# Kernel tuning notes

Measured on AMD Instinct MI355X. Metric: run time of the kernel, lower is better.

## Reference

```python
import jax, jax.numpy as jnp
import numpy as np

B, T, S, H, V, E = 32, 256, 32, 512, 128, 512


def setup_inputs() -> dict:
    key = jax.random.key(0)
    ks = jax.random.split(key, 20)
    f = lambda i, shape: jax.random.normal(ks[i], shape, jnp.float32) * 0.05
    return dict(
        embedding=f(0, (V, H)),
        scope_enc=f(1, (B, S, H)),
        spec_enc=f(2, (B, E)),
        W_init=f(3, (H, E)), b_init=jnp.zeros((H,), jnp.float32),
        W_ih=f(4, (3 * H, 2 * H)), W_hh=f(5, (3 * H, H)),
        b_ih=jnp.zeros((3 * H,), jnp.float32), b_hh=jnp.zeros((3 * H,), jnp.float32),
        W_out=f(6, (V, H)), b_out=jnp.zeros((V,), jnp.float32),
        Wd=f(7, (H, H)), We=f(8, (H, H)), v_attn=f(9, (H,)),
        tokens_in=jax.random.randint(ks[10], (B, T), 0, V),
        tokens_out=jax.random.randint(ks[11], (B, T), 0, V),
        pointer_ids=jax.random.randint(ks[12], (B, T), 0, S),
        ptr_targets=jax.random.randint(ks[13], (B, T), 0, S),
        pointer_mask=jax.random.bernoulli(ks[14], 0.25, (B, T)),
    )


def _gru(x_proj, h0, W_hh, b_hh):
    # x_proj: [B,T,3H] precomputed input projection; torch GRU gate order (r,z,n)
    def step(h, xp):
        gh = h @ W_hh.T + b_hh
        xr, xz, xn = jnp.split(xp, 3, axis=-1)
        hr, hz, hn = jnp.split(gh, 3, axis=-1)
        r = jax.nn.sigmoid(xr + hr)
        z = jax.nn.sigmoid(xz + hz)
        n = jnp.tanh(xn + r * hn)
        h_new = (1.0 - z) * n + z * h
        return h_new, h_new
    _, outs = jax.lax.scan(step, h0, jnp.swapaxes(x_proj, 0, 1))
    return jnp.swapaxes(outs, 0, 1)  # [B,T,H]


def reference(embedding, scope_enc, spec_enc, W_init, b_init, W_ih, W_hh, b_ih, b_hh,
              W_out, b_out, Wd, We, v_attn,
              tokens_in, tokens_out, pointer_ids, ptr_targets, pointer_mask):
    h0 = spec_enc @ W_init.T + b_init                      # initialState
    x_emb = embedding[tokens_in]                           # [B,T,H]
    obj = jax.vmap(lambda s, i: s[i])(scope_enc, pointer_ids)  # [B,T,H]
    obj = jnp.where(pointer_mask[:, :, None], obj, 0.0)    # objectInputs (zeros for non-pointers)
    x = jnp.concatenate([x_emb, obj], axis=-1)             # [B,T,2H]
    x_proj = x @ W_ih.T + b_ih                             # [B,T,3H]
    o = _gru(x_proj, h0, W_hh, b_hh)                       # decoder states [B,T,H]

    # token log-likelihood: -nll_loss(log_softmax(output(o)), targets), summed
    logp = jax.nn.log_softmax(o @ W_out.T + b_out, axis=-1)
    tok_ll = jnp.take_along_axis(logp, tokens_out[:, :, None], axis=-1)[..., 0].sum(-1)

    # pointer attention: additive attention with tanh, log_softmax over scope
    hd = o @ Wd.T                                          # decoderToPointer [B,T,H]
    ok = scope_enc @ We.T                                  # encoderToPointer [B,S,H]
    att = jnp.tanh(hd[:, :, None, :] + ok[:, None, :, :]) @ v_attn  # [B,T,S]
    logatt = jax.nn.log_softmax(att, axis=-1)
    ptr_ll = jnp.take_along_axis(logatt, ptr_targets[:, :, None], axis=-1)[..., 0]
    ptr_ll = jnp.where(pointer_mask, ptr_ll, 0.0).sum(-1)

    return tok_ll + ptr_ll  # per-program likelihood [B]
```

## Files before the change

### kernel.cpp

```cpp
#include <hip/hip_runtime.h>
#include <stdint.h>

#define NB 32
#define NT 256
#define NS 32
#define NH 512
#define NV 128
#define BT 8192

typedef __attribute__((ext_vector_type(8))) __bf16 bf16x8;
typedef __attribute__((ext_vector_type(4))) float f32x4;
typedef __attribute__((ext_vector_type(2))) _Float16 half2v;
typedef unsigned long long u64;

typedef __attribute__((address_space(1))) const unsigned int GASU;
typedef __attribute__((address_space(3))) unsigned int LASU;
#define ASYNC16(g, l) __builtin_amdgcn_global_load_lds((GASU*)(g), (LASU*)(l), 16, 0, 0)

__device__ __forceinline__ half2v pkrtz(float a, float b){
  return __builtin_bit_cast(half2v, __builtin_amdgcn_cvt_pkrtz(a, b));
}
__device__ __forceinline__ unsigned short f2bf(float f){
  unsigned int u = __builtin_bit_cast(unsigned int, f);
  u += 0x7fffu + ((u >> 16) & 1u);
  return (unsigned short)(u >> 16);
}
__device__ __forceinline__ float bf2f(unsigned short h){
  return __builtin_bit_cast(float, ((unsigned int)h) << 16);
}
__device__ __forceinline__ float fexp(float x){ return __builtin_amdgcn_exp2f(x * 1.4426950408889634f); }
__device__ __forceinline__ float fsigm(float x){ return __builtin_amdgcn_rcpf(1.f + fexp(-x)); }
__device__ __forceinline__ float ftanh(float x){
  float t = __builtin_amdgcn_exp2f(x * 2.8853900817779268f);
  return (t - 1.f) * __builtin_amdgcn_rcpf(t + 1.f);
}
__device__ __forceinline__ float flog(float x){ return __builtin_amdgcn_logf(x) * 0.6931471805599453f; }

__device__ __forceinline__ void st_l2(u64* p, u64 v){
  asm volatile("global_store_dwordx2 %0, %1, off" :: "v"(p), "v"(v) : "memory");
}

#define BAR() do{ \
  asm volatile("s_waitcnt lgkmcnt(0)" ::: "memory"); \
  __builtin_amdgcn_sched_barrier(0); \
  __builtin_amdgcn_s_barrier(); \
  __builtin_amdgcn_sched_barrier(0); \
}while(0)

__global__ void k_prep(const float* __restrict__ emb, const float* __restrict__ scope,
                       const float* __restrict__ Wih, const float* __restrict__ Wout,
                       const float* __restrict__ Wd,  const float* __restrict__ We,
                       unsigned short* e_o, unsigned short* s_o, unsigned short* wi_o,
                       unsigned short* wo_o, unsigned short* wd_o, unsigned short* we_o,
                       u64* hx, u64* hxL, float* out, unsigned short* zbuf){
  int g = blockIdx.x*256 + threadIdx.x, gs = gridDim.x*256;
  if (g < 2*NB*256){
    hx[g] = 0ull;
    __hip_atomic_store(hxL + g, 0ull, __ATOMIC_RELAXED, __HIP_MEMORY_SCOPE_AGENT);
  }
  if (g < NB) out[g] = 0.f;
  if (g < 2048) zbuf[g] = 0;
  for (int i=g; i<NV*NH;      i+=gs) e_o[i]  = f2bf(emb[i]);
  for (int i=g; i<NB*NS*NH;   i+=gs) s_o[i]  = f2bf(scope[i]);
  for (int i=g; i<3*NH*2*NH;  i+=gs) wi_o[i] = f2bf(Wih[i]);
  for (int i=g; i<NV*NH;      i+=gs) wo_o[i] = f2bf(Wout[i]);
  for (int i=g; i<NH*NH;      i+=gs) wd_o[i] = f2bf(Wd[i]);
  for (int i=g; i<NH*NH;      i+=gs) we_o[i] = f2bf(We[i]);
}

__global__ void k_h0(const float* __restrict__ spec, const float* __restrict__ Winit,
                     const float* __restrict__ binit, float* __restrict__ h032,
                     u64* __restrict__ hx, u64* __restrict__ hxL){
  const int b = blockIdx.x, tid = threadIdx.x, lane = tid & 63, w = tid >> 6;
  __shared__ float sp[NH];
  __shared__ float hres[NH];
  if (tid < 128) *(float4*)&sp[tid*4] = *(const float4*)(spec + b*NH + tid*4);
  __syncthreads();
  for (int i = 0; i < 128; ++i){
    int j = w * 128 + i;
    const float4* wr = (const float4*)(Winit + (size_t)j * NH);
    float4 x0 = wr[lane*2], x1 = wr[lane*2 + 1];
    float p = x0.x*sp[lane*8]   + x0.y*sp[lane*8+1] + x0.z*sp[lane*8+2] + x0.w*sp[lane*8+3]
            + x1.x*sp[lane*8+4] + x1.y*sp[lane*8+5] + x1.z*sp[lane*8+6] + x1.w*sp[lane*8+7];
    #pragma unroll
    for (int o = 1; o < 64; o <<= 1) p += __shfl_xor(p, o);
    if (lane == 0){
      float v = p + binit[j];
      h032[b*NH + j] = v;
      hres[j] = v;
    }
  }
  __syncthreads();
  if (tid < 256){
    unsigned int pw = __builtin_bit_cast(unsigned int, pkrtz(hres[2*tid], hres[2*tid+1]));
    u64 pv = (1ull << 32) | (u64)pw;
    __hip_atomic_store(hx + b*256 + tid, pv, __ATOMIC_RELAXED, __HIP_MEMORY_SCOPE_AGENT);
    __hip_atomic_store(hxL + b*256 + tid, pv, __ATOMIC_RELAXED, __HIP_MEMORY_SCOPE_AGENT);
  }
}

struct GatherArgs {
  const int* tok; const int* pid; const int* msk;
  const unsigned short* emb; const unsigned short* scope; const unsigned short* zbuf;
};

template<int ASRC>
__global__ __launch_bounds__(256, 2) void k_gemm(
    const unsigned short* __restrict__ A, const unsigned short* __restrict__ Bw,
    float* __restrict__ Cf, unsigned short* __restrict__ Cbf,
    const float* __restrict__ bias, int M, int N, int K, GatherArgs ga)
{
  __shared__ unsigned short lA[2][128][64];
  __shared__ unsigned short lB[2][128][64];
  const int tid = threadIdx.x, lane = tid & 63, wv = tid >> 6;
  const int m0 = blockIdx.x * 128, n0 = blockIdx.y * 128;

  const unsigned short* srcA[4];
  const unsigned short* srcO[4];
  const unsigned short* srcB[4];
  #pragma unroll
  for (int i = 0; i < 4; ++i){
    int ar = m0 + wv*32 + i*8 + (lane >> 3);
    int chunk = (lane & 7) * 8;
    if (ASRC == 0){
      srcA[i] = A + (size_t)ar * K + chunk;
      srcO[i] = nullptr;
    } else {
      int tk = ga.tok[ar], pd = ga.pid[ar], mk = ga.msk[ar];
      srcA[i] = ga.emb + (size_t)tk * NH + chunk;
      srcO[i] = mk ? (ga.scope + ((size_t)((ar >> 8) * NS + pd)) * NH + chunk)
                   : (ga.zbuf + chunk);
    }
    int br = n0 + wv*32 + i*8 + (lane >> 3);
    srcB[i] = Bw + (size_t)br * K + chunk;
  }

  f32x4 acc[4][4];
  #pragma unroll
  for (int x=0;x<4;++x)
    #pragma unroll
    for (int y=0;y<4;++y) acc[x][y] = (f32x4){0.f,0.f,0.f,0.f};

  auto STAGE = [&](int bf, int kt){
    const int k0 = kt * 64;
    #pragma unroll
    for (int i = 0; i < 4; ++i){
      const unsigned short* pa;
      if (ASRC == 0) pa = srcA[i] + k0;
      else pa = (k0 < NH) ? (srcA[i] + k0) : (srcO[i] + (k0 - NH));
      ASYNC16(pa, &lA[bf][wv*32 + i*8][0]);
      ASYNC16(srcB[i] + k0, &lB[bf][wv*32 + i*8][0]);
    }
  };

  STAGE(0, 0);
  asm volatile("s_waitcnt vmcnt(0)" ::: "memory");
  __syncthreads();

  const int wm = (wv >> 1) * 64, wn = (wv & 1) * 64;
  const int fr = lane & 15, fq = lane >> 4;
  const int nt = K >> 6;
  int cur = 0;
  for (int kt = 0; kt < nt; ++kt){
    if (kt + 1 < nt) STAGE(cur ^ 1, kt + 1);
    #pragma unroll
    for (int ks = 0; ks < 2; ++ks){
      bf16x8 af[4], bfv[4];
      #pragma unroll
      for (int mi = 0; mi < 4; ++mi)
        af[mi] = *(const bf16x8*)&lA[cur][wm + mi*16 + fr][ks*32 + fq*8];
      #pragma unroll
      for (int ni = 0; ni < 4; ++ni)
        bfv[ni] = *(const bf16x8*)&lB[cur][wn + ni*16 + fr][ks*32 + fq*8];
      #pragma unroll
      for (int mi = 0; mi < 4; ++mi)
        #pragma unroll
        for (int ni = 0; ni < 4; ++ni)
          acc[mi][ni] = __builtin_amdgcn_mfma_f32_16x16x32_bf16(af[mi], bfv[ni], acc[mi][ni], 0, 0, 0);
    }
    asm volatile("s_waitcnt vmcnt(0)" ::: "memory");
    __syncthreads();
    cur ^= 1;
  }

  #pragma unroll
  for (int mi = 0; mi < 4; ++mi){
    #pragma unroll
    for (int ni = 0; ni < 4; ++ni){
      int col = n0 + wn + ni*16 + fr;
      float bv = bias ? bias[col] : 0.f;
      #pragma unroll
      for (int rr = 0; rr < 4; ++rr){
        int row = m0 + wm + mi*16 + fq*4 + rr;
        float v = acc[mi][ni][rr] + bv;
        if (Cbf) Cbf[(size_t)row * N + col] = f2bf(v);
        else     Cf [(size_t)row * N + col] = v;
      }
    }
  }
}

__global__ __launch_bounds__(512, 1) void k_gru(
    const float* __restrict__ Whh, const float* __restrict__ bhh,
    const unsigned short* __restrict__ xp,
    const float* __restrict__ h032,
    u64* __restrict__ hx,
    u64* __restrict__ hxL,
    unsigned short* __restrict__ obf)
{
  const int bid = blockIdx.x;
  const int b = bid & 31, s = bid >> 5;
  const int tid = threadIdx.x;
  const int u = tid >> 3, r = tid & 7;
  const int jg = s * 64 + u;

  __shared__ __align__(16) unsigned int hl[256];
  __shared__ float xpl[192];
  __shared__ unsigned int pkb[32];

  half2v w0[8][4], w1[8][4], w2[8][4];
  #pragma unroll
  for (int c = 0; c < 8; ++c){
    const int kb = r*64 + ((c + r) & 7) * 8;
    const float* p0 = Whh + ((size_t)(       jg)) * NH + kb;
    const float* p1 = Whh + ((size_t)(  NH + jg)) * NH + kb;
    const float* p2 = Whh + ((size_t)(2*NH + jg)) * NH + kb;
    #pragma unroll
    for (int p = 0; p < 4; ++p){
      float2 a = *(const float2*)(p0 + 2*p);
      float2 c2 = *(const float2*)(p1 + 2*p);
      float2 d = *(const float2*)(p2 + 2*p);
      w0[c][p] = pkrtz(a.x, a.y);
      w1[c][p] = pkrtz(c2.x, c2.y);
      w2[c][p] = pkrtz(d.x, d.y);
    }
  }
  const float bh0 = bhh[jg], bh1 = bhh[NH + jg], bh2 = bhh[2*NH + jg];
  float hprev = h032[b*NH + jg];

  unsigned short xpv = 0;
  if (tid >= 256 && tid < 448){
    int idx = tid - 256;
    xpv = xp[((size_t)(b*NT + 0)) * 1536 + (idx >> 6) * NH + s*64 + (idx & 63)];
  }
  __syncthreads();

  for (int t = 0; t < NT; ++t){
    if (tid < 256){
      const int base = (((t & 1) * NB + b) << 8) + tid;
      const u64* pL = hxL + base;
      const u64* pM = hx + base;
      const unsigned int want = (unsigned int)(t + 1);
      u64 v;
      u64 a  = __hip_atomic_load(pL, __ATOMIC_RELAXED, __HIP_MEMORY_SCOPE_AGENT);
      u64 b2 = __hip_atomic_load(pL, __ATOMIC_RELAXED, __HIP_MEMORY_SCOPE_AGENT);
      int it = 0;
      while (true){
        if ((unsigned int)(a >> 32) == want){ v = a; break; }
        a = b2;
        b2 = __hip_atomic_load(pL, __ATOMIC_RELAXED, __HIP_MEMORY_SCOPE_AGENT);
        if (((++it) & 7) == 0){
          u64 m = __hip_atomic_load(pM, __ATOMIC_RELAXED, __HIP_MEMORY_SCOPE_AGENT);
          if ((unsigned int)(m >> 32) == want){ v = m; break; }
        }
      }
      hl[tid] = (unsigned int)v;
    } else if (tid < 448){
      int idx = tid - 256;
      xpl[idx] = bf2f(xpv);
      if (t + 1 < NT)
        xpv = xp[((size_t)(b*NT + t + 1)) * 1536 + (idx >> 6) * NH + s*64 + (idx & 63)];
    }
    BAR();

    float a0 = 0.f, a1 = 0.f, a2 = 0.f;
    half2v hch[8][4];
    #pragma unroll
    for (int c = 0; c < 8; ++c){
      const int g = (r << 3) + ((c + r) & 7);
      uint4 hv = *(const uint4*)&hl[g * 4];
      hch[c][0] = __builtin_bit_cast(half2v, hv.x);
      hch[c][1] = __builtin_bit_cast(half2v, hv.y);
      hch[c][2] = __builtin_bit_cast(half2v, hv.z);
      hch[c][3] = __builtin_bit_cast(half2v, hv.w);
    }
    #pragma unroll
    for (int c = 0; c < 8; ++c){
      #pragma unroll
      for (int p = 0; p < 4; ++p){
        a0 = __builtin_amdgcn_fdot2(w0[c][p], hch[c][p], a0, false);
        a1 = __builtin_amdgcn_fdot2(w1[c][p], hch[c][p], a1, false);
        a2 = __builtin_amdgcn_fdot2(w2[c][p], hch[c][p], a2, false);
      }
    }
    a0 += __shfl_xor(a0, 1); a0 += __shfl_xor(a0, 2); a0 += __shfl_xor(a0, 4);
    a1 += __shfl_xor(a1, 1); a1 += __shfl_xor(a1, 2); a1 += __shfl_xor(a1, 4);
    a2 += __shfl_xor(a2, 1); a2 += __shfl_xor(a2, 2); a2 += __shfl_xor(a2, 4);

    float hnew = 0.f;
    if (r == 0){
      float xr = xpl[u], xz = xpl[64 + u], xn = xpl[128 + u];
      float rg = fsigm(xr + a0 + bh0);
      float zg = fsigm(xz + a1 + bh1);
      float ng = ftanh(xn + rg * (a2 + bh2));
      hnew = (1.f - zg) * ng + zg * hprev;
      hprev = hnew;
    }
    float hpart = __shfl_xor(hnew, 8);
    if (r == 0 && (u & 1) == 0){
      unsigned int pw = __builtin_bit_cast(unsigned int, pkrtz(hnew, hpart));
      u64 pv = ((u64)(unsigned int)(t + 2) << 32) | (u64)pw;
      const int dst = ((((t + 1) & 1) * NB + b) << 8) + (s << 5) + (u >> 1);
      st_l2(hxL + dst, pv);
      __hip_atomic_store(hx + dst, pv,
                         __ATOMIC_RELAXED, __HIP_MEMORY_SCOPE_AGENT);
      pkb[u >> 1] = (unsigned int)f2bf(hnew) | ((unsigned int)f2bf(hpart) << 16);
    }
    BAR();

    if (tid >= 448 && tid < 480){
      int i = tid - 448;
      ((unsigned int*)obf)[((size_t)(b*NT + t)) * (NH/2) + s*32 + i] = pkb[i];
    }
  }
}

__global__ void k_tokll(const float* __restrict__ logits, const int* __restrict__ tko,
                        float* __restrict__ out){
  const int tid = threadIdx.x, lane = tid & 63, w = tid >> 6;
  const int r0 = blockIdx.x * 64 + w * 16;
  const int b = r0 >> 8;
  int mytok = 0; float tval = 0.f;
  if (lane < 16){
    mytok = tko[r0 + lane];
    tval = logits[(size_t)(r0 + lane) * NV + mytok];
  }
  float acc = 0.f;
  for (int i = 0; i < 16; ++i){
    const float* L = logits + (size_t)(r0 + i) * NV;
    float l0 = L[lane], l1 = L[64 + lane];
    float m = fmaxf(l0, l1);
    #pragma unroll
    for (int o = 1; o < 64; o <<= 1) m = fmaxf(m, __shfl_xor(m, o));
    float sm = fexp(l0 - m) + fexp(l1 - m);
    #pragma unroll
    for (int o = 1; o < 64; o <<= 1) sm += __shfl_xor(sm, o);
    float lse = m + flog(sm);
    float tv = __shfl(tval, i);
    if (lane == 0) acc += tv - lse;
  }
  if (lane == 0) atomicAdd(out + b, acc);
}

__global__ __launch_bounds__(256, 2) void k_ptr(
    const unsigned short* __restrict__ hd, const float* __restrict__ okp,
    const float* __restrict__ vat, const int* __restrict__ ptg,
    const int* __restrict__ pmask, float* __restrict__ out)
{
  __shared__ unsigned short okl[NS][518];
  __shared__ unsigned short hdl[16][518];
  __shared__ float vl[NH];
  __shared__ float attl[16][33];
  const int tid = threadIdx.x;
  const int b = blockIdx.x >> 4, t0 = (blockIdx.x & 15) * 16;
  for (int ii = 0; ii < 64; ++ii){
    int lin = ii*256 + tid;
    int s = lin >> 9, h = lin & 511;
    okl[s][h] = f2bf(okp[((size_t)(b*NS + s)) * NH + h]);
  }
  for (int ii = 0; ii < 32; ++ii){
    int lin = ii*256 + tid;
    int tt = lin >> 9, h = lin & 511;
    hdl[tt][h] = hd[((size_t)(b*NT + t0 + tt)) * NH + h];
  }
  vl[tid] = vat[tid]; vl[256 + tid] = vat[256 + tid];
  __syncthreads();
  #pragma unroll
  for (int pp = 0; pp < 2; ++pp){
    int p = pp*256 + tid;
    int tt = p >> 5, s = p & 31;
    float a = 0.f;
    #pragma unroll 4
    for (int h = 0; h < NH; ++h)
      a += vl[h] * ftanh(bf2f(hdl[tt][h]) + bf2f(okl[s][h]));
    attl[tt][s] = a;
  }
  __syncthreads();
  if (tid < 16){
    int tt = tid;
    float m = -1e30f;
    for (int s = 0; s < NS; ++s) m = fmaxf(m, attl[tt][s]);
    float sm = 0.f;
    for (int s = 0; s < NS; ++s) sm += fexp(attl[tt][s] - m);
    float lse = m + flog(sm);
    int g = b*NT + t0 + tt;
    float c = pmask[g] ? (attl[tt][ptg[g]] - lse) : 0.f;
    #pragma unroll
    for (int o = 1; o < 16; o <<= 1) c += __shfl_xor(c, o);
    if (tid == 0) atomicAdd(out + b, c);
  }
}

extern "C" void kernel_launch(void* const* d_in, const int* in_sizes, int n_in,
                              void* d_out, int out_size, void* d_ws, size_t ws_size,
                              hipStream_t stream)
{
  (void)in_sizes; (void)n_in; (void)out_size; (void)ws_size;
  const float* embedding  = (const float*)d_in[0];
  const float* scope_enc  = (const float*)d_in[1];
  const float* spec_enc   = (const float*)d_in[2];
  const float* W_init     = (const float*)d_in[3];
  const float* b_init     = (const float*)d_in[4];
  const float* W_ih       = (const float*)d_in[5];
  const float* W_hh       = (const float*)d_in[6];
  const float* b_ih       = (const float*)d_in[7];
  const float* b_hh       = (const float*)d_in[8];
  const float* W_out      = (const float*)d_in[9];
  const float* b_out      = (const float*)d_in[10];
  const float* Wd         = (const float*)d_in[11];
  const float* We         = (const float*)d_in[12];
  const float* v_attn     = (const float*)d_in[13];
  const int* tokens_in    = (const int*)d_in[14];
  const int* tokens_out   = (const int*)d_in[15];
  const int* pointer_ids  = (const int*)d_in[16];
  const int* ptr_targets  = (const int*)d_in[17];
  const int* pointer_mask = (const int*)d_in[18];
  float* outF = (float*)d_out;

  uint8_t* wp = (uint8_t*)d_ws;
  auto carve = [&](size_t bytes)->void*{
    void* p = (void*)wp; wp += (bytes + 255) & ~(size_t)255; return p;
  };
  unsigned short* xp_bf    = (unsigned short*)carve((size_t)BT*1536*2);
  unsigned short* o_bf     = (unsigned short*)carve((size_t)BT*NH*2);
  float*          logitsF  = (float*)carve((size_t)BT*NV*4);
  unsigned short* hd_bf    = (unsigned short*)carve((size_t)BT*NH*2);
  float*          okp      = (float*)carve((size_t)NB*NS*NH*4);
  unsigned short* emb_bf   = (unsigned short*)carve((size_t)NV*NH*2);
  unsigned short* scope_bf = (unsigned short*)carve((size_t)NB*NS*NH*2);
  unsigned short* Wih_bf   = (unsigned short*)carve((size_t)3*NH*2*NH*2);
  unsigned short* Wout_bf  = (unsigned short*)carve((size_t)NV*NH*2);
  unsigned short* Wd_bf    = (unsigned short*)carve((size_t)NH*NH*2);
  unsigned short* We_bf    = (unsigned short*)carve((size_t)NH*NH*2);
  float*          h032     = (float*)carve((size_t)NB*NH*4);
  u64*            hx       = (u64*)carve((size_t)2*NB*256*8);
  u64*            hxL      = (u64*)carve((size_t)2*NB*256*8);
  unsigned short* zbuf     = (unsigned short*)carve(4096);

  hipLaunchKernelGGL(k_prep, dim3(1024), dim3(256), 0, stream,
                     embedding, scope_enc, W_ih, W_out, Wd, We,
                     emb_bf, scope_bf, Wih_bf, Wout_bf, Wd_bf, We_bf,
                     hx, hxL, outF, zbuf);
  hipLaunchKernelGGL(k_h0, dim3(NB), dim3(256), 0, stream, spec_enc, W_init, b_init,
                     h032, hx, hxL);
  GatherArgs ga{tokens_in, pointer_ids, pointer_mask, emb_bf, scope_bf, zbuf};
  GatherArgs g0{nullptr,nullptr,nullptr,nullptr,nullptr,nullptr};
  hipLaunchKernelGGL((k_gemm<1>), dim3(64,12), dim3(256), 0, stream,
                     (const unsigned short*)nullptr, Wih_bf, (float*)nullptr, xp_bf,
                     b_ih, BT, 1536, 1024, ga);
  hipLaunchKernelGGL(k_gru, dim3(256), dim3(512), 0, stream,
                     W_hh, b_hh, xp_bf, h032, hx, hxL, o_bf);
  hipLaunchKernelGGL((k_gemm<0>), dim3(64,1), dim3(256), 0, stream,
                     o_bf, Wout_bf, logitsF, (unsigned short*)nullptr, b_out, BT, NV, NH, g0);
  hipLaunchKernelGGL((k_gemm<0>), dim3(64,4), dim3(256), 0, stream,
                     o_bf, Wd_bf, (float*)nullptr, hd_bf, (const float*)nullptr, BT, NH, NH, g0);
  hipLaunchKernelGGL((k_gemm<0>), dim3(8,4), dim3(256), 0, stream,
                     scope_bf, We_bf, okp, (unsigned short*)nullptr, (const float*)nullptr,
                     NB*NS, NH, NH, g0);
  hipLaunchKernelGGL(k_tokll, dim3(128), dim3(256), 0, stream, logitsF, tokens_out, outF);
  hipLaunchKernelGGL(k_ptr, dim3(512), dim3(256), 0, stream,
                     hd_bf, okp, v_attn, ptr_targets, pointer_mask, outF);
}
```

Measured before the change: 646.0 us.

## Fuse input-projection GEMM into GRU kernel with per-row-block ready flags

Merges the gathered input-projection GEMM and the GRU recurrence into one persistent launch. Blocks 0-255 run the GRU and blocks 256+ compute xp tiles, using producer/consumer warp specialisation inside each tile. GRU blocks spin on per-row-block ready counters, so each batch can start once its first half of timesteps is projected, and it waits for the second half at t=127. This aims to hide the GEMM behind the recurrence and drop a launch boundary. It relies on all 1024 blocks being co-resident, otherwise spinning GRU blocks could starve the GEMM blocks and deadlock.

Measured after the change: 803.6 us. 1.24x slower.

```diff
diff --git a/kernel.cpp b/kernel.cpp
--- a/kernel.cpp
+++ b/kernel.cpp
@@ -47,17 +47,23 @@
   __builtin_amdgcn_sched_barrier(0); \
 }while(0)
 
+struct GatherArgs {
+  const int* tok; const int* pid; const int* msk;
+  const unsigned short* emb; const unsigned short* scope; const unsigned short* zbuf;
+};
+
 __global__ void k_prep(const float* __restrict__ emb, const float* __restrict__ scope,
                        const float* __restrict__ Wih, const float* __restrict__ Wout,
                        const float* __restrict__ Wd,  const float* __restrict__ We,
                        unsigned short* e_o, unsigned short* s_o, unsigned short* wi_o,
                        unsigned short* wo_o, unsigned short* wd_o, unsigned short* we_o,
-                       u64* hx, u64* hxL, float* out, unsigned short* zbuf){
+                       u64* hx, u64* hxL, int* ready, float* out, unsigned short* zbuf){
   int g = blockIdx.x*256 + threadIdx.x, gs = gridDim.x*256;
   if (g < 2*NB*256){
     hx[g] = 0ull;
     __hip_atomic_store(hxL + g, 0ull, __ATOMIC_RELAXED, __HIP_MEMORY_SCOPE_AGENT);
   }
+  if (g < 128) __hip_atomic_store(ready + g, 0, __ATOMIC_RELAXED, __HIP_MEMORY_SCOPE_AGENT);
   if (g < NB) out[g] = 0.f;
   if (g < 2048) zbuf[g] = 0;
   for (int i=g; i<NV*NH;      i+=gs) e_o[i]  = f2bf(emb[i]);
@@ -99,124 +105,125 @@
   }
 }
 
-struct GatherArgs {
-  const int* tok; const int* pid; const int* msk;
-  const unsigned short* emb; const unsigned short* scope; const unsigned short* zbuf;
-};
-
-template<int ASRC>
-__global__ __launch_bounds__(256, 2) void k_gemm(
-    const unsigned short* __restrict__ A, const unsigned short* __restrict__ Bw,
-    float* __restrict__ Cf, unsigned short* __restrict__ Cbf,
-    const float* __restrict__ bias, int M, int N, int K, GatherArgs ga)
+__global__ __launch_bounds__(512, 4) void k_main(
+    const float* __restrict__ Whh, const float* __restrict__ bhh,
+    unsigned short* __restrict__ xp,
+    const float* __restrict__ h032,
+    u64* __restrict__ hx, u64* __restrict__ hxL,
+    unsigned short* __restrict__ obf,
+    const unsigned short* __restrict__ Wih,
+    const float* __restrict__ bih,
+    GatherArgs ga, int* __restrict__ ready)
 {
   __shared__ unsigned short lA[2][128][64];
   __shared__ unsigned short lB[2][128][64];
-  const int tid = threadIdx.x, lane = tid & 63, wv = tid >> 6;
-  const int m0 = blockIdx.x * 128, n0 = blockIdx.y * 128;
-
-  const unsigned short* srcA[4];
-  const unsigned short* srcO[4];
-  const unsigned short* srcB[4];
-  #pragma unroll
-  for (int i = 0; i < 4; ++i){
-    int ar = m0 + wv*32 + i*8 + (lane >> 3);
-    int chunk = (lane & 7) * 8;
-    if (ASRC == 0){
-      srcA[i] = A + (size_t)ar * K + chunk;
-      srcO[i] = nullptr;
-    } else {
-      int tk = ga.tok[ar], pd = ga.pid[ar], mk = ga.msk[ar];
-      srcA[i] = ga.emb + (size_t)tk * NH + chunk;
-      srcO[i] = mk ? (ga.scope + ((size_t)((ar >> 8) * NS + pd)) * NH + chunk)
-                   : (ga.zbuf + chunk);
-    }
-    int br = n0 + wv*32 + i*8 + (lane >> 3);
-    srcB[i] = Bw + (size_t)br * K + chunk;
-  }
-
-  f32x4 acc[4][4];
-  #pragma unroll
-  for (int x=0;x<4;++x)
-    #pragma unroll
-    for (int y=0;y<4;++y) acc[x][y] = (f32x4){0.f,0.f,0.f,0.f};
-
-  auto STAGE = [&](int bf, int kt){
-    const int k0 = kt * 64;
-    #pragma unroll
-    for (int i = 0; i < 4; ++i){
-      const unsigned short* pa;
-      if (ASRC == 0) pa = srcA[i] + k0;
-      else pa = (k0 < NH) ? (srcA[i] + k0) : (srcO[i] + (k0 - NH));
-      ASYNC16(pa, &lA[bf][wv*32 + i*8][0]);
-      ASYNC16(srcB[i] + k0, &lB[bf][wv*32 + i*8][0]);
-    }
-  };
-
-  STAGE(0, 0);
-  asm volatile("s_waitcnt vmcnt(0)" ::: "memory");
-  __syncthreads();
-
-  const int wm = (wv >> 1) * 64, wn = (wv & 1) * 64;
-  const int fr = lane & 15, fq = lane >> 4;
-  const int nt = K >> 6;
-  int cur = 0;
-  for (int kt = 0; kt < nt; ++kt){
-    if (kt + 1 < nt) STAGE(cur ^ 1, kt + 1);
-    #pragma unroll
-    for (int ks = 0; ks < 2; ++ks){
-      bf16x8 af[4], bfv[4];
-      #pragma unroll
-      for (int mi = 0; mi < 4; ++mi)
-        af[mi] = *(const bf16x8*)&lA[cur][wm + mi*16 + fr][ks*32 + fq*8];
-      #pragma unroll
-      for (int ni = 0; ni < 4; ++ni)
-        bfv[ni] = *(const bf16x8*)&lB[cur][wn + ni*16 + fr][ks*32 + fq*8];
-      #pragma unroll
-      for (int mi = 0; mi < 4; ++mi)
-        #pragma unroll
-        for (int ni = 0; ni < 4; ++ni)
-          acc[mi][ni] = __builtin_amdgcn_mfma_f32_16x16x32_bf16(af[mi], bfv[ni], acc[mi][ni], 0, 0, 0);
-    }
-    asm volatile("s_waitcnt vmcnt(0)" ::: "memory");
-    __syncthreads();
-    cur ^= 1;
-  }
-
-  #pragma unroll
-  for (int mi = 0; mi < 4; ++mi){
-    #pragma unroll
-    for (int ni = 0; ni < 4; ++ni){
-      int col = n0 + wn + ni*16 + fr;
-      float bv = bias ? bias[col] : 0.f;
-      #pragma unroll
-      for (int rr = 0; rr < 4; ++rr){
-        int row = m0 + wm + mi*16 + fq*4 + rr;
-        float v = acc[mi][ni][rr] + bv;
-        if (Cbf) Cbf[(size_t)row * N + col] = f2bf(v);
-        else     Cf [(size_t)row * N + col] = v;
-      }
-    }
-  }
-}
-
-__global__ __launch_bounds__(512, 1) void k_gru(
-    const float* __restrict__ Whh, const float* __restrict__ bhh,
-    const unsigned short* __restrict__ xp,
-    const float* __restrict__ h032,
-    u64* __restrict__ hx,
-    u64* __restrict__ hxL,
-    unsigned short* __restrict__ obf)
-{
-  const int bid = blockIdx.x;
-  const int b = bid & 31, s = bid >> 5;
-  const int tid = threadIdx.x;
-  const int u = tid >> 3, r = tid & 7;
-  const int jg = s * 64 + u;
-
   __shared__ __align__(16) unsigned int hl[256];
   __shared__ float xpl[192];
   __shared__ unsigned int pkb[32];
+  __shared__ int gDone;
+
+  const int bid = blockIdx.x;
+  const int tid = threadIdx.x;
+  const int lane = tid & 63;
+
+  if (bid >= 256){
+    const int tile = bid - 256;
+    const int rbo = tile / 12, colb = tile - rbo * 12;
+    const int rb = (rbo < 32) ? (rbo << 1) : (((rbo - 32) << 1) | 1);
+    const int m0 = rb << 7, n0 = colb << 7;
+    const int wva = tid >> 6;
+    if (tid == 0) gDone = 0;
+    __syncthreads();
+
+    if (wva >= 4){
+      const int wv = wva - 4;
+      const unsigned short *sA[4], *sO[4], *sB[4];
+      #pragma unroll
+      for (int i = 0; i < 4; ++i){
+        int ar = m0 + wv*32 + i*8 + (lane >> 3);
+        int ch = (lane & 7) * 8;
+        int tk = ga.tok[ar], pd = ga.pid[ar], mk = ga.msk[ar];
+        sA[i] = ga.emb + (size_t)tk * NH + ch;
+        sO[i] = mk ? (ga.scope + ((size_t)((ar >> 8) * NS + pd)) * NH + ch)
+                   : (ga.zbuf + ch);
+        int br = n0 + wv*32 + i*8 + (lane >> 3);
+        sB[i] = Wih + (size_t)br * 1024 + ch;
+      }
+      auto STG = [&](int bf, int kt){
+        const int k0 = kt << 6;
+        #pragma unroll
+        for (int i = 0; i < 4; ++i){
+          const unsigned short* pa = (k0 < NH) ? (sA[i] + k0) : (sO[i] + (k0 - NH));
+          ASYNC16(pa, &lA[bf][wv*32 + i*8][0]);
+          ASYNC16(sB[i] + k0, &lB[bf][wv*32 + i*8][0]);
+        }
+      };
+      STG(0, 0);
+      asm volatile("s_waitcnt vmcnt(0)" ::: "memory");
+      __syncthreads();
+      int cur = 0;
+      for (int kt = 0; kt < 16; ++kt){
+        if (kt < 15) STG(cur ^ 1, kt + 1);
+        asm volatile("s_waitcnt vmcnt(0)" ::: "memory");
+        __syncthreads();
+        cur ^= 1;
+      }
+    } else {
+      f32x4 acc[4][4];
+      #pragma unroll
+      for (int x=0;x<4;++x)
+        #pragma unroll
+        for (int y=0;y<4;++y) acc[x][y] = (f32x4){0.f,0.f,0.f,0.f};
+      __syncthreads();
+      const int wm = (wva >> 1) * 64, wn = (wva & 1) * 64;
+      const int fr = lane & 15, fq = lane >> 4;
+      int cur = 0;
+      for (int kt = 0; kt < 16; ++kt){
+        #pragma unroll
+        for (int ks = 0; ks < 2; ++ks){
+          bf16x8 af[4], bfv[4];
+          #pragma unroll
+          for (int mi = 0; mi < 4; ++mi)
+            af[mi] = *(const bf16x8*)&lA[cur][wm + mi*16 + fr][ks*32 + fq*8];
+          #pragma unroll
+          for (int ni = 0; ni < 4; ++ni)
+            bfv[ni] = *(const bf16x8*)&lB[cur][wn + ni*16 + fr][ks*32 + fq*8];
+          #pragma unroll
+          for (int mi = 0; mi < 4; ++mi)
+            #pragma unroll
+            for (int ni = 0; ni < 4; ++ni)
+              acc[mi][ni] = __builtin_amdgcn_mfma_f32_16x16x32_bf16(af[mi], bfv[ni], acc[mi][ni], 0, 0, 0);
+        }
+        __syncthreads();
+        cur ^= 1;
+      }
+      #pragma unroll
+      for (int mi = 0; mi < 4; ++mi){
+        #pragma unroll
+        for (int ni = 0; ni < 4; ++ni){
+          int col = n0 + wn + ni*16 + fr;
+          float bv = bih[col];
+          #pragma unroll
+          for (int rr = 0; rr < 4; ++rr){
+            int row = m0 + wm + mi*16 + fq*4 + rr;
+            xp[(size_t)row * 1536 + col] = f2bf(acc[mi][ni][rr] + bv);
+          }
+        }
+      }
+      asm volatile("s_waitcnt vmcnt(0)" ::: "memory");
+    }
+    if (lane == 0){
+      if (atomicAdd(&gDone, 1) == 7){
+        __threadfence();
+        atomicAdd(ready + rb, 1);
+      }
+    }
+    return;
+  }
+
+  const int b = bid & 31, s = bid >> 5;
+  const int u = tid >> 3, r = tid & 7;
+  const int jg = s * 64 + u;
 
   half2v w0[8][4], w1[8][4], w2[8][4];
   #pragma unroll
@@ -237,6 +244,12 @@
   }
   const float bh0 = bhh[jg], bh1 = bhh[NH + jg], bh2 = bhh[2*NH + jg];
   float hprev = h032[b*NH + jg];
+
+  if (tid == 0){
+    while (__hip_atomic_load(ready + 2*b, __ATOMIC_RELAXED, __HIP_MEMORY_SCOPE_AGENT) < 12)
+      __builtin_amdgcn_s_sleep(2);
+  }
+  __syncthreads();
 
   unsigned short xpv = 0;
   if (tid >= 256 && tid < 448){
@@ -268,6 +281,10 @@
     } else if (tid < 448){
       int idx = tid - 256;
       xpl[idx] = bf2f(xpv);
+      if (t == 127){
+        while (__hip_atomic_load(ready + 2*b + 1, __ATOMIC_RELAXED,
+                                 __HIP_MEMORY_SCOPE_AGENT) < 12) { }
+      }
       if (t + 1 < NT)
         xpv = xp[((size_t)(b*NT + t + 1)) * 1536 + (idx >> 6) * NH + s*64 + (idx & 63)];
     }
@@ -321,6 +338,90 @@
     if (tid >= 448 && tid < 480){
       int i = tid - 448;
       ((unsigned int*)obf)[((size_t)(b*NT + t)) * (NH/2) + s*32 + i] = pkb[i];
+    }
+  }
+}
+
+template<int ASRC>
+__global__ __launch_bounds__(256, 2) void k_gemm(
+    const unsigned short* __restrict__ A, const unsigned short* __restrict__ Bw,
+    float* __restrict__ Cf, unsigned short* __restrict__ Cbf,
+    const float* __restrict__ bias, int M, int N, int K, GatherArgs ga)
+{
+  __shared__ unsigned short lA[2][128][64];
+  __shared__ unsigned short lB[2][128][64];
+  const int tid = threadIdx.x, lane = tid & 63, wv = tid >> 6;
+  const int m0 = blockIdx.x * 128, n0 = blockIdx.y * 128;
+
+  const unsigned short* srcA[4];
+  const unsigned short* srcB[4];
+  #pragma unroll
+  for (int i = 0; i < 4; ++i){
+    int ar = m0 + wv*32 + i*8 + (lane >> 3);
+    int chunk = (lane & 7) * 8;
+    srcA[i] = A + (size_t)ar * K + chunk;
+    int br = n0 + wv*32 + i*8 + (lane >> 3);
+    srcB[i] = Bw + (size_t)br * K + chunk;
+  }
+
+  f32x4 acc[4][4];
+  #pragma unroll
+  for (int x=0;x<4;++x)
+    #pragma unroll
+    for (int y=0;y<4;++y) acc[x][y] = (f32x4){0.f,0.f,0.f,0.f};
+
+  auto STAGE = [&](int bf, int kt){
+    const int k0 = kt * 64;
+    #pragma unroll
+    for (int i = 0; i < 4; ++i){
+      ASYNC16(srcA[i] + k0, &lA[bf][wv*32 + i*8][0]);
+      ASYNC16(srcB[i] + k0, &lB[bf][wv*32 + i*8][0]);
+    }
+  };
+
+  STAGE(0, 0);
+  asm volatile("s_waitcnt vmcnt(0)" ::: "memory");
+  __syncthreads();
+
+  const int wm = (wv >> 1) * 64, wn = (wv & 1) * 64;
+  const int fr = lane & 15, fq = lane >> 4;
+  const int nt = K >> 6;
+  int cur = 0;
+  for (int kt = 0; kt < nt; ++kt){
+    if (kt + 1 < nt) STAGE(cur ^ 1, kt + 1);
+    #pragma unroll
+    for (int ks = 0; ks < 2; ++ks){
+      bf16x8 af[4], bfv[4];
+      #pragma unroll
+      for (int mi = 0; mi < 4; ++mi)
+        af[mi] = *(const bf16x8*)&lA[cur][wm + mi*16 + fr][ks*32 + fq*8];
+      #pragma unroll
+      for (int ni = 0; ni < 4; ++ni)
+        bfv[ni] = *(const bf16x8*)&lB[cur][wn + ni*16 + fr][ks*32 + fq*8];
+      #pragma unroll
+      for (int mi = 0; mi < 4; ++mi)
+        #pragma unroll
+        for (int ni = 0; ni < 4; ++ni)
+          acc[mi][ni] = __builtin_amdgcn_mfma_f32_16x16x32_bf16(af[mi], bfv[ni], acc[mi][ni], 0, 0, 0);
+    }
+    asm volatile("s_waitcnt vmcnt(0)" ::: "memory");
+    __syncthreads();
+    cur ^= 1;
+  }
+
+  #pragma unroll
+  for (int mi = 0; mi < 4; ++mi){
+    #pragma unroll
+    for (int ni = 0; ni < 4; ++ni){
+      int col = n0 + wn + ni*16 + fr;
+      float bv = bias ? bias[col] : 0.f;
+      #pragma unroll
+      for (int rr = 0; rr < 4; ++rr){
+        int row = m0 + wm + mi*16 + fq*4 + rr;
+        float v = acc[mi][ni][rr] + bv;
+        if (Cbf) Cbf[(size_t)row * N + col] = f2bf(v);
+        else     Cf [(size_t)row * N + col] = v;
+      }
     }
   }
 }
@@ -445,21 +546,19 @@
   float*          h032     = (float*)carve((size_t)NB*NH*4);
   u64*            hx       = (u64*)carve((size_t)2*NB*256*8);
   u64*            hxL      = (u64*)carve((size_t)2*NB*256*8);
+  int*            ready    = (int*)carve(1024);
   unsigned short* zbuf     = (unsigned short*)carve(4096);
 
   hipLaunchKernelGGL(k_prep, dim3(1024), dim3(256), 0, stream,
                      embedding, scope_enc, W_ih, W_out, Wd, We,
                      emb_bf, scope_bf, Wih_bf, Wout_bf, Wd_bf, We_bf,
-                     hx, hxL, outF, zbuf);
+                     hx, hxL, ready, outF, zbuf);
   hipLaunchKernelGGL(k_h0, dim3(NB), dim3(256), 0, stream, spec_enc, W_init, b_init,
                      h032, hx, hxL);
   GatherArgs ga{tokens_in, pointer_ids, pointer_mask, emb_bf, scope_bf, zbuf};
   GatherArgs g0{nullptr,nullptr,nullptr,nullptr,nullptr,nullptr};
-  hipLaunchKernelGGL((k_gemm<1>), dim3(64,12), dim3(256), 0, stream,
-                     (const unsigned short*)nullptr, Wih_bf, (float*)nullptr, xp_bf,
-                     b_ih, BT, 1536, 1024, ga);
-  hipLaunchKernelGGL(k_gru, dim3(256), dim3(512), 0, stream,
-                     W_hh, b_hh, xp_bf, h032, hx, hxL, o_bf);
+  hipLaunchKernelGGL(k_main, dim3(1024), dim3(512), 0, stream,
+                     W_hh, b_hh, xp_bf, h032, hx, hxL, o_bf, Wih_bf, b_ih, ga, ready);
   hipLaunchKernelGGL((k_gemm<0>), dim3(64,1), dim3(256), 0, stream,
                      o_bf, Wout_bf, logitsF, (unsigned short*)nullptr, b_out, BT, NV, NH, g0);
   hipLaunchKernelGGL((k_gemm<0>), dim3(64,4), dim3(256), 0, stream,
```

## Precompute input projections per vocab row and scope row instead of per token

Applied to the files above, without the earlier changes.

The input projection x @ W_ih^T is split into an embedding part and a pointer-object part. Each part is projected once over the small tables (128 vocab rows and 1024 scope rows), replacing the 8192-row gathered GEMM. The GRU kernel then gathers the projected rows per timestep by token and pointer id and adds them, using the mask to drop the object term. This removes a large GEMM and its 8192x1536 intermediate, but adds two dependent index loads and an extra add per step inside the latency-critical recurrence.

Result: faster. 596.6 us (-7.6%).

```diff
diff --git a/kernel.cpp b/kernel.cpp
--- a/kernel.cpp
+++ b/kernel.cpp
@@ -52,14 +52,13 @@
                        const float* __restrict__ Wd,  const float* __restrict__ We,
                        unsigned short* e_o, unsigned short* s_o, unsigned short* wi_o,
                        unsigned short* wo_o, unsigned short* wd_o, unsigned short* we_o,
-                       u64* hx, u64* hxL, float* out, unsigned short* zbuf){
+                       u64* hx, u64* hxL, float* out){
   int g = blockIdx.x*256 + threadIdx.x, gs = gridDim.x*256;
   if (g < 2*NB*256){
     hx[g] = 0ull;
     __hip_atomic_store(hxL + g, 0ull, __ATOMIC_RELAXED, __HIP_MEMORY_SCOPE_AGENT);
   }
   if (g < NB) out[g] = 0.f;
-  if (g < 2048) zbuf[g] = 0;
   for (int i=g; i<NV*NH;      i+=gs) e_o[i]  = f2bf(emb[i]);
   for (int i=g; i<NB*NS*NH;   i+=gs) s_o[i]  = f2bf(scope[i]);
   for (int i=g; i<3*NH*2*NH;  i+=gs) wi_o[i] = f2bf(Wih[i]);
@@ -99,16 +98,10 @@
   }
 }
 
-struct GatherArgs {
-  const int* tok; const int* pid; const int* msk;
-  const unsigned short* emb; const unsigned short* scope; const unsigned short* zbuf;
-};
-
-template<int ASRC>
 __global__ __launch_bounds__(256, 2) void k_gemm(
     const unsigned short* __restrict__ A, const unsigned short* __restrict__ Bw,
     float* __restrict__ Cf, unsigned short* __restrict__ Cbf,
-    const float* __restrict__ bias, int M, int N, int K, GatherArgs ga)
+    const float* __restrict__ bias, int M, int N, int K, int ldb)
 {
   __shared__ unsigned short lA[2][128][64];
   __shared__ unsigned short lB[2][128][64];
@@ -116,23 +109,14 @@
   const int m0 = blockIdx.x * 128, n0 = blockIdx.y * 128;
 
   const unsigned short* srcA[4];
-  const unsigned short* srcO[4];
   const unsigned short* srcB[4];
   #pragma unroll
   for (int i = 0; i < 4; ++i){
     int ar = m0 + wv*32 + i*8 + (lane >> 3);
     int chunk = (lane & 7) * 8;
-    if (ASRC == 0){
-      srcA[i] = A + (size_t)ar * K + chunk;
-      srcO[i] = nullptr;
-    } else {
-      int tk = ga.tok[ar], pd = ga.pid[ar], mk = ga.msk[ar];
-      srcA[i] = ga.emb + (size_t)tk * NH + chunk;
-      srcO[i] = mk ? (ga.scope + ((size_t)((ar >> 8) * NS + pd)) * NH + chunk)
-                   : (ga.zbuf + chunk);
-    }
+    srcA[i] = A + (size_t)ar * K + chunk;
     int br = n0 + wv*32 + i*8 + (lane >> 3);
-    srcB[i] = Bw + (size_t)br * K + chunk;
+    srcB[i] = Bw + (size_t)br * ldb + chunk;
   }
 
   f32x4 acc[4][4];
@@ -145,10 +129,7 @@
     const int k0 = kt * 64;
     #pragma unroll
     for (int i = 0; i < 4; ++i){
-      const unsigned short* pa;
-      if (ASRC == 0) pa = srcA[i] + k0;
-      else pa = (k0 < NH) ? (srcA[i] + k0) : (srcO[i] + (k0 - NH));
-      ASYNC16(pa, &lA[bf][wv*32 + i*8][0]);
+      ASYNC16(srcA[i] + k0, &lA[bf][wv*32 + i*8][0]);
       ASYNC16(srcB[i] + k0, &lB[bf][wv*32 + i*8][0]);
     }
   };
@@ -202,7 +183,10 @@
 
 __global__ __launch_bounds__(512, 1) void k_gru(
     const float* __restrict__ Whh, const float* __restrict__ bhh,
-    const unsigned short* __restrict__ xp,
+    const unsigned short* __restrict__ embp,
+    const unsigned short* __restrict__ objp,
+    const int* __restrict__ tokin, const int* __restrict__ pids,
+    const int* __restrict__ pmask,
     const float* __restrict__ h032,
     u64* __restrict__ hx,
     u64* __restrict__ hxL,
@@ -238,10 +222,16 @@
   const float bh0 = bhh[jg], bh1 = bhh[NH + jg], bh2 = bhh[2*NH + jg];
   float hprev = h032[b*NH + jg];
 
-  unsigned short xpv = 0;
+  unsigned short xe = 0, xo = 0; int mk = 0;
+  int jcol = 0;
   if (tid >= 256 && tid < 448){
     int idx = tid - 256;
-    xpv = xp[((size_t)(b*NT + 0)) * 1536 + (idx >> 6) * NH + s*64 + (idx & 63)];
+    jcol = (idx >> 6) * NH + s*64 + (idx & 63);
+    int tk = tokin[b*NT + 0];
+    int pd = pids [b*NT + 0];
+    mk     = pmask[b*NT + 0];
+    xe = embp[(size_t)tk * 1536 + jcol];
+    xo = objp[((size_t)(b*NS + pd)) * 1536 + jcol];
   }
   __syncthreads();
 
@@ -267,9 +257,14 @@
       hl[tid] = (unsigned int)v;
     } else if (tid < 448){
       int idx = tid - 256;
-      xpl[idx] = bf2f(xpv);
-      if (t + 1 < NT)
-        xpv = xp[((size_t)(b*NT + t + 1)) * 1536 + (idx >> 6) * NH + s*64 + (idx & 63)];
+      xpl[idx] = bf2f(xe) + (mk ? bf2f(xo) : 0.f);
+      if (t + 1 < NT){
+        int tk = tokin[b*NT + t + 1];
+        int pd = pids [b*NT + t + 1];
+        mk     = pmask[b*NT + t + 1];
+        xe = embp[(size_t)tk * 1536 + jcol];
+        xo = objp[((size_t)(b*NS + pd)) * 1536 + jcol];
+      }
     }
     BAR();
 
@@ -431,7 +426,8 @@
   auto carve = [&](size_t bytes)->void*{
     void* p = (void*)wp; wp += (bytes + 255) & ~(size_t)255; return p;
   };
-  unsigned short* xp_bf    = (unsigned short*)carve((size_t)BT*1536*2);
+  unsigned short* embp_bf  = (unsigned short*)carve((size_t)NV*1536*2);
+  unsigned short* objp_bf  = (unsigned short*)carve((size_t)NB*NS*1536*2);
   unsigned short* o_bf     = (unsigned short*)carve((size_t)BT*NH*2);
   float*          logitsF  = (float*)carve((size_t)BT*NV*4);
   unsigned short* hd_bf    = (unsigned short*)carve((size_t)BT*NH*2);
@@ -445,28 +441,31 @@
   float*          h032     = (float*)carve((size_t)NB*NH*4);
   u64*            hx       = (u64*)carve((size_t)2*NB*256*8);
   u64*            hxL      = (u64*)carve((size_t)2*NB*256*8);
-  unsigned short* zbuf     = (unsigned short*)carve(4096);
 
   hipLaunchKernelGGL(k_prep, dim3(1024), dim3(256), 0, stream,
                      embedding, scope_enc, W_ih, W_out, Wd, We,
                      emb_bf, scope_bf, Wih_bf, Wout_bf, Wd_bf, We_bf,
-                     hx, hxL, outF, zbuf);
+                     hx, hxL, outF);
   hipLaunchKernelGGL(k_h0, dim3(NB), dim3(256), 0, stream, spec_enc, W_init, b_init,
                      h032, hx, hxL);
-  GatherArgs ga{tokens_in, pointer_ids, pointer_mask, emb_bf, scope_bf, zbuf};
-  GatherArgs g0{nullptr,nullptr,nullptr,nullptr,nullptr,nullptr};
-  hipLaunchKernelGGL((k_gemm<1>), dim3(64,12), dim3(256), 0, stream,
-                     (const unsigned short*)nullptr, Wih_bf, (float*)nullptr, xp_bf,
-                     b_ih, BT, 1536, 1024, ga);
+  hipLaunchKernelGGL(k_gemm, dim3(1,12), dim3(256), 0, stream,
+                     emb_bf, Wih_bf, (float*)nullptr, embp_bf,
+                     b_ih, NV, 1536, NH, 1024);
+  hipLaunchKernelGGL(k_gemm, dim3(8,12), dim3(256), 0, stream,
+                     scope_bf, Wih_bf + NH, (float*)nullptr, objp_bf,
+                     (const float*)nullptr, NB*NS, 1536, NH, 1024);
   hipLaunchKernelGGL(k_gru, dim3(256), dim3(512), 0, stream,
-                     W_hh, b_hh, xp_bf, h032, hx, hxL, o_bf);
-  hipLaunchKernelGGL((k_gemm<0>), dim3(64,1), dim3(256), 0, stream,
-                     o_bf, Wout_bf, logitsF, (unsigned short*)nullptr, b_out, BT, NV, NH, g0);
-  hipLaunchKernelGGL((k_gemm<0>), dim3(64,4), dim3(256), 0, stream,
-                     o_bf, Wd_bf, (float*)nullptr, hd_bf, (const float*)nullptr, BT, NH, NH, g0);
-  hipLaunchKernelGGL((k_gemm<0>), dim3(8,4), dim3(256), 0, stream,
-                     scope_bf, We_bf, okp, (unsigned short*)nullptr, (const float*)nullptr,
-                     NB*NS, NH, NH, g0);
+                     W_hh, b_hh, embp_bf, objp_bf, tokens_in, pointer_ids,
+                     pointer_mask, h032, hx, hxL, o_bf);
+  hipLaunchKernelGGL(k_gemm, dim3(64,1), dim3(256), 0, stream,
+                     o_bf, Wout_bf, logitsF, (unsigned short*)nullptr, b_out,
+                     BT, NV, NH, NH);
+  hipLaunchKernelGGL(k_gemm, dim3(64,4), dim3(256), 0, stream,
+                     o_bf, Wd_bf, (float*)nullptr, hd_bf, (const float*)nullptr,
+                     BT, NH, NH, NH);
+  hipLaunchKernelGGL(k_gemm, dim3(8,4), dim3(256), 0, stream,
+                     scope_bf, We_bf, okp, (unsigned short*)nullptr,
+                     (const float*)nullptr, NB*NS, NH, NH, NH);
   hipLaunchKernelGGL(k_tokll, dim3(128), dim3(256), 0, stream, logitsF, tokens_out, outF);
   hipLaunchKernelGGL(k_ptr, dim3(512), dim3(256), 0, stream,
                      hd_bf, okp, v_attn, ptr_targets, pointer_mask, outF);
```
